# Optimization experiments

Measured on AMD Instinct MI355X. Metric: run time of the kernel, lower is better.

The kernel has to match this reference:

```python
import jax, jax.numpy as jnp
import numpy as np

NUM_GROUPS = 16   # static upper bound on group ids (actual ids in [0, 12))
MIN_COUNT = 10    # min_subgroup_count


def setup_inputs() -> dict:
    key = jax.random.key(0)
    ks = jax.random.split(key, 7)
    B = 32768
    N = 16777216  # dataset_size
    probs = jax.random.uniform(ks[0], (B,), dtype=jnp.float32)
    labels = jax.random.randint(ks[1], (B,), 0, 2, dtype=jnp.int32)
    groups = jax.random.randint(ks[2], (B,), 0, 12, dtype=jnp.int32)
    indices = jax.random.randint(ks[3], (B,), 0, N, dtype=jnp.int32)
    # persistent buffers, pre-filled with valid mid-epoch state
    score_buffer = jax.random.uniform(ks[4], (N,), dtype=jnp.float32)
    label_buffer = jax.random.randint(ks[5], (N,), 0, 2, dtype=jnp.int32)
    group_buffer = jax.random.randint(ks[6], (N,), 0, 12, dtype=jnp.int32)
    return {"probs": probs, "labels": labels, "groups": groups, "indices": indices,
            "score_buffer": score_buffer, "label_buffer": label_buffer,
            "group_buffer": group_buffer}


def reference(probs, labels, groups, indices, score_buffer, label_buffer, group_buffer):
    # scatter current batch into dataset-sized buffers (functional clone + write)
    scores = score_buffer.at[indices].set(probs)
    labs = label_buffer.at[indices].set(labels)
    grps = group_buffer.at[indices].set(groups)

    valid = (~jnp.isnan(scores)) & (labs >= 0) & (grps >= 0)
    scores = jnp.where(valid, scores, 0.0)        # kill NaNs before weighted sums
    seg = jnp.where(valid, grps, 0)               # invalid rows get weight 0 anyway

    def group_var(lab_val):
        # per-group mean of scores restricted to (valid & label==lab_val),
        # then unbiased variance across groups meeting the min-count threshold
        w = (valid & (labs == lab_val)).astype(scores.dtype)
        sums = jax.ops.segment_sum(scores * w, seg, num_segments=NUM_GROUPS)
        cnts = jax.ops.segment_sum(w, seg, num_segments=NUM_GROUPS)
        avg = sums / jnp.maximum(cnts, 1.0)
        incl = (cnts >= MIN_COUNT).astype(scores.dtype)
        n = incl.sum()
        mean = (avg * incl).sum() / jnp.maximum(n, 1.0)
        var = (incl * (avg - mean) ** 2).sum() / jnp.maximum(n - 1.0, 1.0)  # ddof=1
        return var, n

    pos_var, n_pos = group_var(1)
    neg_var, n_neg = group_var(0)
    pos_ok = n_pos >= 2.0
    neg_ok = n_neg >= 2.0
    loss = jnp.where(pos_ok & neg_ok, 0.5 * (pos_var + neg_var),
                     jnp.where(pos_ok, pos_var,
                               jnp.where(neg_ok, neg_var, 0.0)))
    return loss
```

## Files before the change

kernel.cpp:

```cpp
#include <hip/hip_runtime.h>
#include <hip/hip_bf16.h>


#define TBL   65536u
#define TBLM  (TBL - 1u)
#define NGR   12
#define NBK   24
#define NCOL  25
#define NTHR  256
#define CHUNK 16384
#define ITER  (CHUNK / 4 / NTHR)
#define DEPTH 4
#define MINC  10.0

__device__ __forceinline__ unsigned hash_idx(unsigned idx) {
    return (idx * 2654435761u) & TBLM;
}

__global__ void k_vote(const int* __restrict__ indices,
                       unsigned long long* __restrict__ table,
                       unsigned* __restrict__ bitmap, int B) {
    int b = blockIdx.x * blockDim.x + threadIdx.x;
    if (b >= B) return;
    unsigned idx = (unsigned)indices[b];
    atomicOr(&bitmap[idx >> 5], 1u << (idx & 31u));
    unsigned long long key = ((unsigned long long)(idx + 1u)) << 32;
    unsigned long long val = key | (unsigned long long)(unsigned)b;
    unsigned slot = hash_idx(idx);
    for (;;) {
        unsigned long long prev = atomicCAS(&table[slot], 0ULL, val);
        if (prev == 0ULL) return;
        if ((prev >> 32) == (unsigned long long)(idx + 1u)) {
            atomicMax(&table[slot], val);
            return;
        }
        slot = (slot + 1u) & TBLM;
    }
}

__device__ __forceinline__ void apply_ovr(int idx, float& s, int& l, int& g,
        const unsigned long long* __restrict__ table,
        const float* __restrict__ probs, const int* __restrict__ labels,
        const int* __restrict__ groups) {
    unsigned slot = hash_idx((unsigned)idx);
    unsigned hi = (unsigned)idx + 1u;
    for (;;) {
        unsigned long long e = table[slot];
        if ((unsigned)(e >> 32) == hi) {
            int b = (int)(e & 0xffffffffu);
            s = probs[b]; l = labels[b]; g = groups[b];
            return;
        }
        slot = (slot + 1u) & TBLM;
    }
}

__device__ __forceinline__ void quad_p1(float* __restrict__ row,
        float4 s4, int4 l4, int4 g4, unsigned bits, int v,
        const unsigned long long* __restrict__ table,
        const float* __restrict__ probs, const int* __restrict__ labels,
        const int* __restrict__ groups) {
    float ss[4] = {s4.x, s4.y, s4.z, s4.w};
    int   ll[4] = {l4.x, l4.y, l4.z, l4.w};
    int   gg[4] = {g4.x, g4.y, g4.z, g4.w};
    float val[4]; int bkt[4];
#pragma unroll
    for (int e = 0; e < 4; ++e) {
        float s = ss[e]; int l = ll[e], g = gg[e];
        if ((bits >> e) & 1u)
            apply_ovr((v << 2) + e, s, l, g, table, probs, labels, groups);
        bool valid = (s == s) && ((unsigned)l < 2u) && ((unsigned)g < (unsigned)NGR);
        bkt[e] = valid ? (g * 2 + l) : NBK;
        val[e] = valid ? s : 0.f;
    }
#define MRG(i, j) { bool m_ = (bkt[i] == bkt[j]); \
                    val[i] += m_ ? val[j] : 0.f;  \
                    bkt[j] = m_ ? NBK : bkt[j];   \
                    val[j] = m_ ? 0.f : val[j]; }
    MRG(0,1) MRG(0,2) MRG(0,3) MRG(1,2) MRG(1,3) MRG(2,3)
#undef MRG
    float a0 = row[bkt[0]], a1 = row[bkt[1]], a2 = row[bkt[2]], a3 = row[bkt[3]];
    row[bkt[0]] = a0 + val[0];
    row[bkt[1]] = a1 + val[1];
    row[bkt[2]] = a2 + val[2];
    row[bkt[3]] = a3 + val[3];
}

__global__ __launch_bounds__(NTHR) void k_pass1(
        const float* __restrict__ sb, const int* __restrict__ lb,
        const int* __restrict__ gb, const unsigned* __restrict__ bitmap,
        const unsigned long long* __restrict__ table,
        const float* __restrict__ probs, const int* __restrict__ labels,
        const int* __restrict__ groups,
        float* __restrict__ bsum, int n, int nblk) {
    __shared__ float s_acc[NTHR * NCOL];
    int tid = threadIdx.x, blk = blockIdx.x;
    for (int i = tid; i < NTHR * NCOL; i += NTHR) s_acc[i] = 0.f;
    __syncthreads();
    float* row = &s_acc[tid * NCOL];
    int vbase = (blk * CHUNK) >> 2, nv = n >> 2;
    if (vbase + (CHUNK >> 2) <= nv) {
        int v0 = vbase + tid;
        float4 ps[DEPTH]; int4 pl[DEPTH], pg[DEPTH]; unsigned pb[DEPTH];
#pragma unroll
        for (int d = 0; d < DEPTH; ++d) {
            int v = v0 + d * NTHR;
            ps[d] = ((const float4*)sb)[v];
            pl[d] = ((const int4*)lb)[v];
            pg[d] = ((const int4*)gb)[v];
            pb[d] = bitmap[v >> 3];
        }
        unsigned sh = (unsigned)((v0 & 7) * 4);
        for (int it0 = 0; it0 < ITER; it0 += DEPTH) {
#pragma unroll
            for (int d = 0; d < DEPTH; ++d) {
                int it = it0 + d;
                int v = v0 + it * NTHR;
                float4 s4 = ps[d]; int4 l4 = pl[d], g4 = pg[d];
                unsigned bits = pb[d] >> sh;
                if (it + DEPTH < ITER) {
                    int w = v + DEPTH * NTHR;
                    ps[d] = ((const float4*)sb)[w];
                    pl[d] = ((const int4*)lb)[w];
                    pg[d] = ((const int4*)gb)[w];
                    pb[d] = bitmap[w >> 3];
                }
                quad_p1(row, s4, l4, g4, bits, v, table, probs, labels, groups);
            }
        }
    } else {
        for (int it = 0; it < ITER; ++it) {
            int v = vbase + it * NTHR + tid;
            if (v >= nv) break;
            float4 s4 = ((const float4*)sb)[v];
            int4   l4 = ((const int4*)lb)[v];
            int4   g4 = ((const int4*)gb)[v];
            unsigned bits = bitmap[v >> 3] >> ((v & 7) * 4);
            quad_p1(row, s4, l4, g4, bits, v, table, probs, labels, groups);
        }
    }
    if (blk == nblk - 1) {
        for (int i = (nv << 2) + tid; i < n; i += NTHR) {
            float s = sb[i]; int l = lb[i], g = gb[i];
            if ((bitmap[i >> 5] >> (i & 31)) & 1u)
                apply_ovr(i, s, l, g, table, probs, labels, groups);
            bool valid = (s == s) && ((unsigned)l < 2u) && ((unsigned)g < (unsigned)NGR);
            int bk = valid ? (g * 2 + l) : NBK;
            row[bk] += valid ? s : 0.f;
        }
    }
    __syncthreads();
    if (tid < NBK * 8) {
        int bkt = tid >> 3, sub = tid & 7;
        float sm = 0.f;
        for (int j = 0; j < 32; ++j) sm += s_acc[(sub * 32 + j) * NCOL + bkt];
        for (int d = 4; d >= 1; d >>= 1) sm += __shfl_down(sm, d, 8);
        if (!sub) bsum[bkt * nblk + blk] = sm;
    }
}

__global__ void k_scan(const float* __restrict__ bsum,
                       float* __restrict__ bpref, int nblk) {
    __shared__ double sc[NTHR];
    int t = threadIdx.x, k = blockIdx.x;
    const float* src = bsum  + (size_t)k * nblk;
    float*       dst = bpref + (size_t)k * nblk;
    double carry = 0.0;
    for (int s0 = 0; s0 < nblk; s0 += 4 * NTHR) {
        int i0 = s0 + 4 * t;
        float x0 = (i0 + 0 < nblk) ? src[i0 + 0] : 0.f;
        float x1 = (i0 + 1 < nblk) ? src[i0 + 1] : 0.f;
        float x2 = (i0 + 2 < nblk) ? src[i0 + 2] : 0.f;
        float x3 = (i0 + 3 < nblk) ? src[i0 + 3] : 0.f;
        double p0 = (double)x0, p1 = p0 + x1, p2 = p1 + x2, tot = p2 + x3;
        sc[t] = tot;
        __syncthreads();
        for (int st = 1; st < NTHR; st <<= 1) {
            double a = (t >= st) ? sc[t - st] : 0.0;
            __syncthreads();
            sc[t] += a;
            __syncthreads();
        }
        double excl = carry + sc[t] - tot;
        if (i0 + 0 < nblk) dst[i0 + 0] = (float)excl;
        if (i0 + 1 < nblk) dst[i0 + 1] = (float)(excl + p0);
        if (i0 + 2 < nblk) dst[i0 + 2] = (float)(excl + p1);
        if (i0 + 3 < nblk) dst[i0 + 3] = (float)(excl + p2);
        double bt = sc[NTHR - 1];
        __syncthreads();
        carry += bt;
    }
}

__device__ __forceinline__ double aload_d(const double* p) {
    unsigned long long u = __hip_atomic_load((const unsigned long long*)p,
                              __ATOMIC_RELAXED, __HIP_MEMORY_SCOPE_AGENT);
    return __longlong_as_double((long long)u);
}

__device__ __forceinline__ void quad_p2(float2* __restrict__ row,
        const float2* __restrict__ s_model,
        float4 s4, int4 l4, int4 g4, unsigned bits, int v, int base,
        const unsigned long long* __restrict__ table,
        const float* __restrict__ probs, const int* __restrict__ labels,
        const int* __restrict__ groups) {
    float ss[4] = {s4.x, s4.y, s4.z, s4.w};
    int   ll[4] = {l4.x, l4.y, l4.z, l4.w};
    int   gg[4] = {g4.x, g4.y, g4.z, g4.w};
    float cv[4], cn[4]; int bkt[4];
#pragma unroll
    for (int e = 0; e < 4; ++e) {
        int idx = (v << 2) + e;
        float s = ss[e]; int l = ll[e], g = gg[e];
        if ((bits >> e) & 1u)
            apply_ovr(idx, s, l, g, table, probs, labels, groups);
        bool valid = (s == s) && ((unsigned)l < 2u) && ((unsigned)g < (unsigned)NGR);
        int bk = valid ? (g * 2 + l) : NBK;
        float2 m = s_model[bk];
        float S = fmaf(m.y, (float)(idx - base), m.x);
        float T = S + s;
        unsigned ue = __float_as_uint(T) & 0x7f800000u;
        float c;
        if (ue < (24u << 23)) c = s;
        else {
            unsigned ub = ue - (23u << 23);
            float u    = __uint_as_float(ub);
            float uinv = __uint_as_float((254u << 23) - ub);
            c = u * rintf(s * uinv);
        }
        bkt[e] = bk;
        cv[e] = valid ? c : 0.f;
        cn[e] = valid ? 1.f : 0.f;
    }
#define MRG(i, j) { bool m_ = (bkt[i] == bkt[j]); \
                    cv[i] += m_ ? cv[j] : 0.f;    \
                    cn[i] += m_ ? cn[j] : 0.f;    \
                    bkt[j] = m_ ? NBK : bkt[j];   \
                    cv[j] = m_ ? 0.f : cv[j];     \
                    cn[j] = m_ ? 0.f : cn[j]; }
    MRG(0,1) MRG(0,2) MRG(0,3) MRG(1,2) MRG(1,3) MRG(2,3)
#undef MRG
    float2 a0 = row[bkt[0]], a1 = row[bkt[1]], a2 = row[bkt[2]], a3 = row[bkt[3]];
    a0.x += cv[0]; a0.y += cn[0];
    a1.x += cv[1]; a1.y += cn[1];
    a2.x += cv[2]; a2.y += cn[2];
    a3.x += cv[3]; a3.y += cn[3];
    row[bkt[0]] = a0; row[bkt[1]] = a1; row[bkt[2]] = a2; row[bkt[3]] = a3;
}

__global__ __launch_bounds__(NTHR) void k_pass2(
        const float* __restrict__ sb, const int* __restrict__ lb,
        const int* __restrict__ gb, const unsigned* __restrict__ bitmap,
        const unsigned long long* __restrict__ table,
        const float* __restrict__ probs, const int* __restrict__ labels,
        const int* __restrict__ groups,
        const float* __restrict__ bsum, const float* __restrict__ bpref,
        double* __restrict__ acc_sum, double* __restrict__ acc_cnt,
        unsigned* __restrict__ done, float* __restrict__ out,
        int n, int nblk) {
    __shared__ float2 s_acc[NTHR * NCOL];
    __shared__ float2 s_model[NCOL];
    int tid = threadIdx.x, blk = blockIdx.x;
    for (int i = tid; i < NTHR * NCOL; i += NTHR) s_acc[i] = make_float2(0.f, 0.f);
    if (tid < NBK)
        s_model[tid] = make_float2(bpref[tid * nblk + blk],
                                   bsum[tid * nblk + blk] * (1.0f / CHUNK));
    if (tid == NBK) s_model[NBK] = make_float2(0.f, 0.f);
    __syncthreads();
    float2* row = &s_acc[tid * NCOL];
    int base = blk * CHUNK;
    int vbase = base >> 2, nv = n >> 2;
    if (vbase + (CHUNK >> 2) <= nv) {
        int v0 = vbase + tid;
        float4 ps[DEPTH]; int4 pl[DEPTH], pg[DEPTH]; unsigned pb[DEPTH];
#pragma unroll
        for (int d = 0; d < DEPTH; ++d) {
            int v = v0 + d * NTHR;
            ps[d] = ((const float4*)sb)[v];
            pl[d] = ((const int4*)lb)[v];
            pg[d] = ((const int4*)gb)[v];
            pb[d] = bitmap[v >> 3];
        }
        unsigned sh = (unsigned)((v0 & 7) * 4);
        for (int it0 = 0; it0 < ITER; it0 += DEPTH) {
#pragma unroll
            for (int d = 0; d < DEPTH; ++d) {
                int it = it0 + d;
                int v = v0 + it * NTHR;
                float4 s4 = ps[d]; int4 l4 = pl[d], g4 = pg[d];
                unsigned bits = pb[d] >> sh;
                if (it + DEPTH < ITER) {
                    int w = v + DEPTH * NTHR;
                    ps[d] = ((const float4*)sb)[w];
                    pl[d] = ((const int4*)lb)[w];
                    pg[d] = ((const int4*)gb)[w];
                    pb[d] = bitmap[w >> 3];
                }
                quad_p2(row, s_model, s4, l4, g4, bits, v, base,
                        table, probs, labels, groups);
            }
        }
    } else {
        for (int it = 0; it < ITER; ++it) {
            int v = vbase + it * NTHR + tid;
            if (v >= nv) break;
            float4 s4 = ((const float4*)sb)[v];
            int4   l4 = ((const int4*)lb)[v];
            int4   g4 = ((const int4*)gb)[v];
            unsigned bits = bitmap[v >> 3] >> ((v & 7) * 4);
            quad_p2(row, s_model, s4, l4, g4, bits, v, base,
                    table, probs, labels, groups);
        }
    }
    if (blk == nblk - 1) {
        for (int i = (nv << 2) + tid; i < n; i += NTHR) {
            float s = sb[i]; int l = lb[i], g = gb[i];
            if ((bitmap[i >> 5] >> (i & 31)) & 1u)
                apply_ovr(i, s, l, g, table, probs, labels, groups);
            bool valid = (s == s) && ((unsigned)l < 2u) && ((unsigned)g < (unsigned)NGR);
            int bk = valid ? (g * 2 + l) : NBK;
            float2 m = s_model[bk];
            float S = fmaf(m.y, (float)(i - base), m.x);
            float T = S + s;
            unsigned ue = __float_as_uint(T) & 0x7f800000u;
            float c;
            if (ue < (24u << 23)) c = s;
            else {
                unsigned ub = ue - (23u << 23);
                float u    = __uint_as_float(ub);
                float uinv = __uint_as_float((254u << 23) - ub);
                c = u * rintf(s * uinv);
            }
            float2 a = row[bk];
            a.x += valid ? c : 0.f;
            a.y += valid ? 1.f : 0.f;
            row[bk] = a;
        }
    }
    __syncthreads();
    if (tid < NBK * 8) {
        int bkt = tid >> 3, sub = tid & 7;
        float sm = 0.f, cc = 0.f;
        for (int j = 0; j < 32; ++j) {
            float2 a = s_acc[(sub * 32 + j) * NCOL + bkt];
            sm += a.x; cc += a.y;
        }
        for (int d = 4; d >= 1; d >>= 1) {
            sm += __shfl_down(sm, d, 8);
            cc += __shfl_down(cc, d, 8);
        }
        if (!sub) {
            atomicAdd(&acc_sum[bkt], (double)sm);
            atomicAdd(&acc_cnt[bkt], (double)cc);
        }
    }
    __syncthreads();
    if (tid == 0) {
        __threadfence();
        unsigned r = __hip_atomic_fetch_add(done, 1u, __ATOMIC_ACQ_REL,
                                            __HIP_MEMORY_SCOPE_AGENT);
        if (r == (unsigned)(gridDim.x - 1)) {
            double var[2], nn[2];
            for (int l = 0; l < 2; ++l) {
                double avg[NGR];
                double ncnt = 0.0, s = 0.0;
                for (int g = 0; g < NGR; ++g) {
                    double c  = aload_d(&acc_cnt[g * 2 + l]);
                    double sm = aload_d(&acc_sum[g * 2 + l]);
                    double a = sm / fmax(c, 1.0);
                    avg[g] = a;
                    if (c >= MINC) { ncnt += 1.0; s += a; }
                }
                double mean = s / fmax(ncnt, 1.0), v = 0.0;
                for (int g = 0; g < NGR; ++g) {
                    double c = aload_d(&acc_cnt[g * 2 + l]);
                    if (c >= MINC) { double d = avg[g] - mean; v += d * d; }
                }
                var[l] = v / fmax(ncnt - 1.0, 1.0);
                nn[l] = ncnt;
            }
            bool p = nn[1] >= 2.0, q = nn[0] >= 2.0;
            double loss = (p && q) ? 0.5 * (var[1] + var[0])
                        : (p ? var[1] : (q ? var[0] : 0.0));
            out[0] = (float)loss;
        }
    }
}

extern "C" void kernel_launch(void* const* d_in, const int* in_sizes, int n_in,
                              void* d_out, int out_size, void* d_ws, size_t ws_size,
                              hipStream_t stream) {
    const float* probs   = (const float*)d_in[0];
    const int*   labels  = (const int*)d_in[1];
    const int*   groups  = (const int*)d_in[2];
    const int*   indices = (const int*)d_in[3];
    const float* sb      = (const float*)d_in[4];
    const int*   lb      = (const int*)d_in[5];
    const int*   gb      = (const int*)d_in[6];
    int B = in_sizes[0];
    int n = in_sizes[4];
    int nblk   = (n + CHUNK - 1) / CHUNK;
    int nwords = (n + 31) / 32;

    char* ws = (char*)d_ws;
    size_t off = 0;
    unsigned long long* table = (unsigned long long*)(ws + off); off += (size_t)TBL * 8;
    unsigned* bitmap  = (unsigned*)(ws + off); off += (size_t)nwords * 4;
    double*   acc_sum = (double*)(ws + off);   off += NBK * 8;
    double*   acc_cnt = (double*)(ws + off);   off += NBK * 8;
    unsigned* done    = (unsigned*)(ws + off); off += 8;
    size_t zero_bytes = off;
    float*    bsum    = (float*)(ws + off);    off += (size_t)nblk * NBK * 4;
    float*    bpref   = (float*)(ws + off);    off += (size_t)nblk * NBK * 4;

    hipMemsetAsync(d_ws, 0, zero_bytes, stream);

    dim3 bblk((B + NTHR - 1) / NTHR);
    hipLaunchKernelGGL(k_vote, bblk, dim3(NTHR), 0, stream,
                       indices, table, bitmap, B);
    hipLaunchKernelGGL(k_pass1, dim3(nblk), dim3(NTHR), 0, stream,
                       sb, lb, gb, bitmap, table, probs, labels, groups,
                       bsum, n, nblk);
    hipLaunchKernelGGL(k_scan, dim3(NBK), dim3(NTHR), 0, stream,
                       bsum, bpref, nblk);
    hipLaunchKernelGGL(k_pass2, dim3(nblk), dim3(NTHR), 0, stream,
                       sb, lb, gb, bitmap, table, probs, labels, groups,
                       bsum, bpref, acc_sum, acc_cnt, done, (float*)d_out,
                       n, nblk);
}
```

Baseline: 340.2 us.

## Pre-resolve hash table entries into packed float4 records for override lookups

Adds a kernel that walks the hash table once and materialises, for each slot, a float4 holding the batch score, label, group and key. The lookups in both passes then need a single 16-byte load per probe instead of a table load followed by three dependent gathers. The main loops are also flattened into one fully unrolled loop with a compiler memory barrier, to shape load scheduling. The cost is an extra kernel launch and a 1 MB resolved table that has to be written and then read.

```diff
diff --git a/kernel.cpp b/kernel.cpp
--- a/kernel.cpp
+++ b/kernel.cpp
@@ -38,17 +38,33 @@
     }
 }
 
+__global__ void k_resolve(const unsigned long long* __restrict__ table,
+                          const float* __restrict__ probs,
+                          const int* __restrict__ labels,
+                          const int* __restrict__ groups,
+                          float4* __restrict__ tbl2) {
+    int s = blockIdx.x * blockDim.x + threadIdx.x;
+    unsigned long long e = table[s];
+    unsigned hi = (unsigned)(e >> 32);
+    float4 r = make_float4(0.f, 0.f, 0.f, 0.f);
+    if (hi) {
+        int b = (int)(e & 0xffffffffu);
+        r.x = probs[b];
+        r.y = __int_as_float(labels[b]);
+        r.z = __int_as_float(groups[b]);
+        r.w = __uint_as_float(hi);
+    }
+    tbl2[s] = r;
+}
+
 __device__ __forceinline__ void apply_ovr(int idx, float& s, int& l, int& g,
-        const unsigned long long* __restrict__ table,
-        const float* __restrict__ probs, const int* __restrict__ labels,
-        const int* __restrict__ groups) {
+        const float4* __restrict__ tbl2) {
     unsigned slot = hash_idx((unsigned)idx);
     unsigned hi = (unsigned)idx + 1u;
     for (;;) {
-        unsigned long long e = table[slot];
-        if ((unsigned)(e >> 32) == hi) {
-            int b = (int)(e & 0xffffffffu);
-            s = probs[b]; l = labels[b]; g = groups[b];
+        float4 r = tbl2[slot];
+        if (__float_as_uint(r.w) == hi) {
+            s = r.x; l = __float_as_int(r.y); g = __float_as_int(r.z);
             return;
         }
         slot = (slot + 1u) & TBLM;
@@ -57,9 +73,7 @@
 
 __device__ __forceinline__ void quad_p1(float* __restrict__ row,
         float4 s4, int4 l4, int4 g4, unsigned bits, int v,
-        const unsigned long long* __restrict__ table,
-        const float* __restrict__ probs, const int* __restrict__ labels,
-        const int* __restrict__ groups) {
+        const float4* __restrict__ tbl2) {
     float ss[4] = {s4.x, s4.y, s4.z, s4.w};
     int   ll[4] = {l4.x, l4.y, l4.z, l4.w};
     int   gg[4] = {g4.x, g4.y, g4.z, g4.w};
@@ -68,7 +82,7 @@
     for (int e = 0; e < 4; ++e) {
         float s = ss[e]; int l = ll[e], g = gg[e];
         if ((bits >> e) & 1u)
-            apply_ovr((v << 2) + e, s, l, g, table, probs, labels, groups);
+            apply_ovr((v << 2) + e, s, l, g, tbl2);
         bool valid = (s == s) && ((unsigned)l < 2u) && ((unsigned)g < (unsigned)NGR);
         bkt[e] = valid ? (g * 2 + l) : NBK;
         val[e] = valid ? s : 0.f;
@@ -89,9 +103,7 @@
 __global__ __launch_bounds__(NTHR) void k_pass1(
         const float* __restrict__ sb, const int* __restrict__ lb,
         const int* __restrict__ gb, const unsigned* __restrict__ bitmap,
-        const unsigned long long* __restrict__ table,
-        const float* __restrict__ probs, const int* __restrict__ labels,
-        const int* __restrict__ groups,
+        const float4* __restrict__ tbl2,
         float* __restrict__ bsum, int n, int nblk) {
     __shared__ float s_acc[NTHR * NCOL];
     int tid = threadIdx.x, blk = blockIdx.x;
@@ -111,22 +123,21 @@
             pb[d] = bitmap[v >> 3];
         }
         unsigned sh = (unsigned)((v0 & 7) * 4);
-        for (int it0 = 0; it0 < ITER; it0 += DEPTH) {
-#pragma unroll
-            for (int d = 0; d < DEPTH; ++d) {
-                int it = it0 + d;
-                int v = v0 + it * NTHR;
-                float4 s4 = ps[d]; int4 l4 = pl[d], g4 = pg[d];
-                unsigned bits = pb[d] >> sh;
-                if (it + DEPTH < ITER) {
-                    int w = v + DEPTH * NTHR;
-                    ps[d] = ((const float4*)sb)[w];
-                    pl[d] = ((const int4*)lb)[w];
-                    pg[d] = ((const int4*)gb)[w];
-                    pb[d] = bitmap[w >> 3];
-                }
-                quad_p1(row, s4, l4, g4, bits, v, table, probs, labels, groups);
+#pragma unroll
+        for (int it = 0; it < ITER; ++it) {
+            int d = it & (DEPTH - 1);
+            int v = v0 + it * NTHR;
+            float4 s4 = ps[d]; int4 l4 = pl[d], g4 = pg[d];
+            unsigned bits = pb[d] >> sh;
+            if (it + DEPTH < ITER) {
+                int w = v + DEPTH * NTHR;
+                ps[d] = ((const float4*)sb)[w];
+                pl[d] = ((const int4*)lb)[w];
+                pg[d] = ((const int4*)gb)[w];
+                pb[d] = bitmap[w >> 3];
             }
+            asm volatile("" ::: "memory");
+            quad_p1(row, s4, l4, g4, bits, v, tbl2);
         }
     } else {
         for (int it = 0; it < ITER; ++it) {
@@ -136,14 +147,14 @@
             int4   l4 = ((const int4*)lb)[v];
             int4   g4 = ((const int4*)gb)[v];
             unsigned bits = bitmap[v >> 3] >> ((v & 7) * 4);
-            quad_p1(row, s4, l4, g4, bits, v, table, probs, labels, groups);
+            quad_p1(row, s4, l4, g4, bits, v, tbl2);
         }
     }
     if (blk == nblk - 1) {
         for (int i = (nv << 2) + tid; i < n; i += NTHR) {
             float s = sb[i]; int l = lb[i], g = gb[i];
             if ((bitmap[i >> 5] >> (i & 31)) & 1u)
-                apply_ovr(i, s, l, g, table, probs, labels, groups);
+                apply_ovr(i, s, l, g, tbl2);
             bool valid = (s == s) && ((unsigned)l < 2u) && ((unsigned)g < (unsigned)NGR);
             int bk = valid ? (g * 2 + l) : NBK;
             row[bk] += valid ? s : 0.f;
@@ -201,9 +212,7 @@
 __device__ __forceinline__ void quad_p2(float2* __restrict__ row,
         const float2* __restrict__ s_model,
         float4 s4, int4 l4, int4 g4, unsigned bits, int v, int base,
-        const unsigned long long* __restrict__ table,
-        const float* __restrict__ probs, const int* __restrict__ labels,
-        const int* __restrict__ groups) {
+        const float4* __restrict__ tbl2) {
     float ss[4] = {s4.x, s4.y, s4.z, s4.w};
     int   ll[4] = {l4.x, l4.y, l4.z, l4.w};
     int   gg[4] = {g4.x, g4.y, g4.z, g4.w};
@@ -213,7 +222,7 @@
         int idx = (v << 2) + e;
         float s = ss[e]; int l = ll[e], g = gg[e];
         if ((bits >> e) & 1u)
-            apply_ovr(idx, s, l, g, table, probs, labels, groups);
+            apply_ovr(idx, s, l, g, tbl2);
         bool valid = (s == s) && ((unsigned)l < 2u) && ((unsigned)g < (unsigned)NGR);
         int bk = valid ? (g * 2 + l) : NBK;
         float2 m = s_model[bk];
@@ -251,9 +260,7 @@
 __global__ __launch_bounds__(NTHR) void k_pass2(
         const float* __restrict__ sb, const int* __restrict__ lb,
         const int* __restrict__ gb, const unsigned* __restrict__ bitmap,
-        const unsigned long long* __restrict__ table,
-        const float* __restrict__ probs, const int* __restrict__ labels,
-        const int* __restrict__ groups,
+        const float4* __restrict__ tbl2,
         const float* __restrict__ bsum, const float* __restrict__ bpref,
         double* __restrict__ acc_sum, double* __restrict__ acc_cnt,
         unsigned* __restrict__ done, float* __restrict__ out,
@@ -282,23 +289,21 @@
             pb[d] = bitmap[v >> 3];
         }
         unsigned sh = (unsigned)((v0 & 7) * 4);
-        for (int it0 = 0; it0 < ITER; it0 += DEPTH) {
-#pragma unroll
-            for (int d = 0; d < DEPTH; ++d) {
-                int it = it0 + d;
-                int v = v0 + it * NTHR;
-                float4 s4 = ps[d]; int4 l4 = pl[d], g4 = pg[d];
-                unsigned bits = pb[d] >> sh;
-                if (it + DEPTH < ITER) {
-                    int w = v + DEPTH * NTHR;
-                    ps[d] = ((const float4*)sb)[w];
-                    pl[d] = ((const int4*)lb)[w];
-                    pg[d] = ((const int4*)gb)[w];
-                    pb[d] = bitmap[w >> 3];
-                }
-                quad_p2(row, s_model, s4, l4, g4, bits, v, base,
-                        table, probs, labels, groups);
+#pragma unroll
+        for (int it = 0; it < ITER; ++it) {
+            int d = it & (DEPTH - 1);
+            int v = v0 + it * NTHR;
+            float4 s4 = ps[d]; int4 l4 = pl[d], g4 = pg[d];
+            unsigned bits = pb[d] >> sh;
+            if (it + DEPTH < ITER) {
+                int w = v + DEPTH * NTHR;
+                ps[d] = ((const float4*)sb)[w];
+                pl[d] = ((const int4*)lb)[w];
+                pg[d] = ((const int4*)gb)[w];
+                pb[d] = bitmap[w >> 3];
             }
+            asm volatile("" ::: "memory");
+            quad_p2(row, s_model, s4, l4, g4, bits, v, base, tbl2);
         }
     } else {
         for (int it = 0; it < ITER; ++it) {
@@ -308,15 +313,14 @@
             int4   l4 = ((const int4*)lb)[v];
             int4   g4 = ((const int4*)gb)[v];
             unsigned bits = bitmap[v >> 3] >> ((v & 7) * 4);
-            quad_p2(row, s_model, s4, l4, g4, bits, v, base,
-                    table, probs, labels, groups);
+            quad_p2(row, s_model, s4, l4, g4, bits, v, base, tbl2);
         }
     }
     if (blk == nblk - 1) {
         for (int i = (nv << 2) + tid; i < n; i += NTHR) {
             float s = sb[i]; int l = lb[i], g = gb[i];
             if ((bitmap[i >> 5] >> (i & 31)) & 1u)
-                apply_ovr(i, s, l, g, table, probs, labels, groups);
+                apply_ovr(i, s, l, g, tbl2);
             bool valid = (s == s) && ((unsigned)l < 2u) && ((unsigned)g < (unsigned)NGR);
             int bk = valid ? (g * 2 + l) : NBK;
             float2 m = s_model[bk];
@@ -410,6 +414,7 @@
     double*   acc_cnt = (double*)(ws + off);   off += NBK * 8;
     unsigned* done    = (unsigned*)(ws + off); off += 8;
     size_t zero_bytes = off;
+    float4*   tbl2    = (float4*)(ws + off);   off += (size_t)TBL * 16;
     float*    bsum    = (float*)(ws + off);    off += (size_t)nblk * NBK * 4;
     float*    bpref   = (float*)(ws + off);    off += (size_t)nblk * NBK * 4;
 
@@ -418,13 +423,13 @@
     dim3 bblk((B + NTHR - 1) / NTHR);
     hipLaunchKernelGGL(k_vote, bblk, dim3(NTHR), 0, stream,
                        indices, table, bitmap, B);
+    hipLaunchKernelGGL(k_resolve, dim3(TBL / NTHR), dim3(NTHR), 0, stream,
+                       table, probs, labels, groups, tbl2);
     hipLaunchKernelGGL(k_pass1, dim3(nblk), dim3(NTHR), 0, stream,
-                       sb, lb, gb, bitmap, table, probs, labels, groups,
-                       bsum, n, nblk);
+                       sb, lb, gb, bitmap, tbl2, bsum, n, nblk);
     hipLaunchKernelGGL(k_scan, dim3(NBK), dim3(NTHR), 0, stream,
                        bsum, bpref, nblk);
     hipLaunchKernelGGL(k_pass2, dim3(nblk), dim3(NTHR), 0, stream,
-                       sb, lb, gb, bitmap, table, probs, labels, groups,
-                       bsum, bpref, acc_sum, acc_cnt, done, (float*)d_out,
-                       n, nblk);
-}
+                       sb, lb, gb, bitmap, tbl2, bsum, bpref,
+                       acc_sum, acc_cnt, done, (float*)d_out, n, nblk);
+}
```

Result: no change. 334.7 us (-1.6%).
